# Kernel optimization log

Hardware: AMD Instinct MI355X
Metric: run time of the kernel (lower is better)

Reference implementation:

```python
import jax, jax.numpy as jnp
import numpy as np

SM_SCALE = 0.07216878364870322  # 1/sqrt(192)
PAGE_SIZE = 64


def setup_inputs() -> dict:
    key = jax.random.key(0)
    ks = jax.random.split(key, 6)
    B, Hq, Hkv = 32, 16, 1
    DN, DR, DV = 128, 64, 128
    NUM_PAGES, MAX_PAGES = 2048, 64
    return {
        "q": jax.random.normal(ks[0], (B, Hq, DN + DR), dtype=jnp.float32),
        "k_nope_buffer": jax.random.normal(ks[1], (NUM_PAGES, PAGE_SIZE, Hkv, DN), dtype=jnp.float32),
        "k_rope_buffer": jax.random.normal(ks[2], (NUM_PAGES, PAGE_SIZE, Hkv, DR), dtype=jnp.float32),
        "v_buffer": jax.random.normal(ks[3], (NUM_PAGES, PAGE_SIZE, Hkv, DV), dtype=jnp.float32),
        "seq_lens": jax.random.randint(ks[4], (B,), 1, MAX_PAGES * PAGE_SIZE + 1, dtype=jnp.int32),
        "block_table": jax.random.randint(ks[5], (B, MAX_PAGES), 0, NUM_PAGES, dtype=jnp.int32),
    }


def reference(q, k_nope_buffer, k_rope_buffer, v_buffer, seq_lens, block_table):
    B, Hq, _ = q.shape
    Hkv = k_nope_buffer.shape[2]
    dn = k_nope_buffer.shape[-1]
    dv = v_buffer.shape[-1]
    max_kv = block_table.shape[1] * PAGE_SIZE

    q_nope = q[:, :, :dn]            # (B, Hq, dn)
    q_rope = q[:, :, dn:]            # (B, Hq, dr)

    # Gather pages per batch: (B, max_pages, page, Hkv, d) -> (B, max_kv, Hkv, d)
    kn = k_nope_buffer[block_table].reshape(B, max_kv, Hkv, dn)
    kr = k_rope_buffer[block_table].reshape(B, max_kv, Hkv, -1)
    v = v_buffer[block_table].reshape(B, max_kv, Hkv, dv)

    rep = Hq // Hkv  # GQA repeat_interleave == repeat along head axis
    if rep != 1:
        kn = jnp.repeat(kn, rep, axis=2)
        kr = jnp.repeat(kr, rep, axis=2)
        v = jnp.repeat(v, rep, axis=2)

    scores = (jnp.einsum('bhd,bkhd->bhk', q_nope, kn)
              + jnp.einsum('bhd,bkhd->bhk', q_rope, kr)).astype(jnp.float32) * SM_SCALE
    # Mask out key positions beyond each sequence length (replaces per-batch slicing)
    valid = jnp.arange(max_kv)[None, None, :] < seq_lens[:, None, None]
    scores = jnp.where(valid, scores, -jnp.inf)
    probs = jax.nn.softmax(scores, axis=-1).astype(v.dtype)  # (B, Hq, max_kv)
    out = jnp.einsum('bhk,bkhd->bhd', probs, v)              # (B, Hq, dv)
    return out
```

## Files before the change

### kernel.cpp

```cpp
#include <hip/hip_runtime.h>
#include <math.h>

#define NB 32
#define HQ 16
#define DN 128
#define DR 64
#define DQ (DN + DR)
#define DV 128
#define PAGE 64
#define MAXP 64
#define SM_SCALE 0.07216878364870322f
#define RS 88

typedef __attribute__((ext_vector_type(8))) _Float16 f16x8;
typedef __attribute__((ext_vector_type(4))) _Float16 f16x4;
typedef __attribute__((ext_vector_type(2))) __fp16   h16x2;
typedef __attribute__((ext_vector_type(4))) float    f32x4;

union F16x8 { f16x8 v; h16x2 h[4]; };
union F16x4 { f16x4 v; h16x2 h[2]; };

#define WAVE_LDS_FENCE() asm volatile("s_waitcnt lgkmcnt(0)" ::: "memory")

template<int NSC>
__global__ __launch_bounds__(64, 1)
void attn_partial_kernel(const float* __restrict__ q,
                         const float* __restrict__ kn,
                         const float* __restrict__ kr,
                         const float* __restrict__ v,
                         const int* __restrict__ seq_lens,
                         const int* __restrict__ block_table,
                         float* __restrict__ o_part,
                         float* __restrict__ ml_part)
{
    const int lane = (int)threadIdx.x;
    const int ln   = lane & 15;
    const int qd   = lane >> 4;

    const int b = blockIdx.x / NSC;
    const int c = blockIdx.x % NSC;

    const int seq = seq_lens[b];
    if (c * PAGE >= seq) return;

    __shared__ _Float16 p_s[HQ][RS];

    F16x8 bq[6];
    {
        const float* qrow = q + ((size_t)b * HQ + ln) * DQ + qd * 8;
        #pragma unroll
        for (int kt = 0; kt < 6; kt++) {
            float4 x0 = *(const float4*)(qrow + kt * 32);
            float4 x1 = *(const float4*)(qrow + kt * 32 + 4);
            bq[kt].h[0] = __builtin_amdgcn_cvt_pkrtz(x0.x, x0.y);
            bq[kt].h[1] = __builtin_amdgcn_cvt_pkrtz(x0.z, x0.w);
            bq[kt].h[2] = __builtin_amdgcn_cvt_pkrtz(x1.x, x1.y);
            bq[kt].h[3] = __builtin_amdgcn_cvt_pkrtz(x1.z, x1.w);
        }
    }

    float m_run = -INFINITY, l_run = 0.f;
    f32x4 o_acc[8];
    #pragma unroll
    for (int i = 0; i < 8; i++) o_acc[i] = (f32x4){0.f, 0.f, 0.f, 0.f};

    #pragma unroll
    for (int pg = 0; pg < MAXP / NSC; pg++) {
        const int page = c + pg * NSC;
        if (page * PAGE >= seq) break;
        const int pid = block_table[b * MAXP + page];

        const float* knb = kn + (size_t)pid * PAGE * DN;
        const float* krb = kr + (size_t)pid * PAGE * DR;
        const float* vb  = v  + (size_t)pid * PAGE * DV;

        f32x4 sc[4];
        #pragma unroll
        for (int mt = 0; mt < 4; mt++) sc[mt] = (f32x4){0.f, 0.f, 0.f, 0.f};
        #pragma unroll
        for (int mt = 0; mt < 4; mt++) {
            const float* rn = knb + (mt * 16 + ln) * DN + qd * 8;
            const float* rr = krb + (mt * 16 + ln) * DR + qd * 8;
            #pragma unroll
            for (int kt = 0; kt < 6; kt++) {
                const float* src = (kt < 4) ? (rn + kt * 32) : (rr + (kt - 4) * 32);
                float4 x0 = *(const float4*)(src);
                float4 x1 = *(const float4*)(src + 4);
                F16x8 a;
                a.h[0] = __builtin_amdgcn_cvt_pkrtz(x0.x, x0.y);
                a.h[1] = __builtin_amdgcn_cvt_pkrtz(x0.z, x0.w);
                a.h[2] = __builtin_amdgcn_cvt_pkrtz(x1.x, x1.y);
                a.h[3] = __builtin_amdgcn_cvt_pkrtz(x1.z, x1.w);
                sc[mt] = __builtin_amdgcn_mfma_f32_16x16x32_f16(a.v, bq[kt].v, sc[mt], 0, 0, 0);
            }
        }

        float vraw[16][8];
        #pragma unroll
        for (int kt2 = 0; kt2 < 2; kt2++) {
            const int t0 = kt2 * 32 + qd * 8;
            #pragma unroll
            for (int mt2 = 0; mt2 < 8; mt2++) {
                const float* vc = vb + mt2 * 16 + ln;
                #pragma unroll
                for (int j = 0; j < 8; j++)
                    vraw[kt2 * 8 + mt2][j] = vc[(size_t)(t0 + j) * DV];
            }
        }

        float sv[4][4];
        float smax = -INFINITY;
        #pragma unroll
        for (int mt = 0; mt < 4; mt++)
            #pragma unroll
            for (int r = 0; r < 4; r++) {
                int tok = page * PAGE + mt * 16 + qd * 4 + r;
                float x = (tok < seq) ? sc[mt][r] * SM_SCALE : -INFINITY;
                sv[mt][r] = x;
                smax = fmaxf(smax, x);
            }
        smax = fmaxf(smax, __shfl_xor(smax, 16));
        smax = fmaxf(smax, __shfl_xor(smax, 32));
        const float m_new = fmaxf(m_run, smax);
        const float alpha = __expf(m_run - m_new);
        m_run = m_new;
        float lsum = 0.f;
        #pragma unroll
        for (int mt = 0; mt < 4; mt++)
            #pragma unroll
            for (int r = 0; r < 4; r++) {
                float e = __expf(sv[mt][r] - m_new);
                sv[mt][r] = e;
                lsum += e;
            }
        lsum += __shfl_xor(lsum, 16);
        lsum += __shfl_xor(lsum, 32);
        l_run = l_run * alpha + lsum;

        WAVE_LDS_FENCE();
        #pragma unroll
        for (int mt = 0; mt < 4; mt++) {
            F16x4 w;
            w.h[0] = __builtin_amdgcn_cvt_pkrtz(sv[mt][0], sv[mt][1]);
            w.h[1] = __builtin_amdgcn_cvt_pkrtz(sv[mt][2], sv[mt][3]);
            *(f16x4*)(&p_s[ln][mt * 16 + qd * 4]) = w.v;
        }
        WAVE_LDS_FENCE();

        #pragma unroll
        for (int i = 0; i < 8; i++) o_acc[i] *= alpha;

        #pragma unroll
        for (int kt2 = 0; kt2 < 2; kt2++) {
            f16x8 pf = *(const f16x8*)(&p_s[ln][kt2 * 32 + qd * 8]);
            #pragma unroll
            for (int mt2 = 0; mt2 < 8; mt2++) {
                const float* vr = vraw[kt2 * 8 + mt2];
                F16x8 a;
                a.h[0] = __builtin_amdgcn_cvt_pkrtz(vr[0], vr[1]);
                a.h[1] = __builtin_amdgcn_cvt_pkrtz(vr[2], vr[3]);
                a.h[2] = __builtin_amdgcn_cvt_pkrtz(vr[4], vr[5]);
                a.h[3] = __builtin_amdgcn_cvt_pkrtz(vr[6], vr[7]);
                o_acc[mt2] = __builtin_amdgcn_mfma_f32_16x16x32_f16(a.v, pf, o_acc[mt2], 0, 0, 0);
            }
        }
    }

    float* op = o_part + ((size_t)(b * NSC + c) * HQ + ln) * DV + qd * 4;
    #pragma unroll
    for (int mt2 = 0; mt2 < 8; mt2++)
        *(f32x4*)(op + mt2 * 16) = o_acc[mt2];
    if (qd == 0) {
        float2* ml = (float2*)(ml_part) + (size_t)(b * NSC + c) * HQ + ln;
        *ml = make_float2(m_run, l_run);
    }
}

template<int NSC>
__global__ __launch_bounds__(128)
void attn_combine_kernel(const float* __restrict__ o_part,
                         const float* __restrict__ ml_part,
                         const int* __restrict__ seq_lens,
                         float* __restrict__ out)
{
    const int h = blockIdx.x;
    const int b = blockIdx.y;
    const int d = (int)threadIdx.x;
    const int seq = seq_lens[b];
    int npages = (seq + PAGE - 1) / PAGE;
    int ns = npages < NSC ? npages : NSC;

    const float2* mlb = (const float2*)(ml_part) + (size_t)b * NSC * HQ + h;
    float M = -INFINITY;
    #pragma unroll 8
    for (int s2 = 0; s2 < ns; s2++)
        M = fmaxf(M, mlb[(size_t)s2 * HQ].x);

    float acc = 0.f, den = 0.f;
    #pragma unroll 4
    for (int s2 = 0; s2 < ns; s2++) {
        float2 ml = mlb[(size_t)s2 * HQ];
        float e = __expf(ml.x - M);
        float o = o_part[((size_t)(b * NSC + s2) * HQ + h) * DV + d];
        acc += e * o;
        den += e * ml.y;
    }
    out[((size_t)b * HQ + h) * DV + d] = acc / den;
}

template<int NSC>
static void launch_all(const float* q, const float* kn, const float* kr,
                       const float* v, const int* seq_lens, const int* block_table,
                       float* d_ws, float* d_out, hipStream_t stream)
{
    float* o_part  = d_ws;
    float* ml_part = o_part + (size_t)NB * NSC * HQ * DV;
    attn_partial_kernel<NSC><<<NB * NSC, 64, 0, stream>>>(
        q, kn, kr, v, seq_lens, block_table, o_part, ml_part);
    attn_combine_kernel<NSC><<<dim3(HQ, NB), 128, 0, stream>>>(
        o_part, ml_part, seq_lens, d_out);
}

extern "C" void kernel_launch(void* const* d_in, const int* in_sizes, int n_in,
                              void* d_out, int out_size, void* d_ws, size_t ws_size,
                              hipStream_t stream)
{
    const float* q  = (const float*)d_in[0];
    const float* kn = (const float*)d_in[1];
    const float* kr = (const float*)d_in[2];
    const float* v  = (const float*)d_in[3];
    const int* seq_lens    = (const int*)d_in[4];
    const int* block_table = (const int*)d_in[5];

    const size_t need64 = (size_t)NB * 64 * HQ * (DV + 2) * 4;
    const size_t need32 = (size_t)NB * 32 * HQ * (DV + 2) * 4;

    if (ws_size >= need64)
        launch_all<64>(q, kn, kr, v, seq_lens, block_table, (float*)d_ws, (float*)d_out, stream);
    else if (ws_size >= need32)
        launch_all<32>(q, kn, kr, v, seq_lens, block_table, (float*)d_ws, (float*)d_out, stream);
    else
        launch_all<16>(q, kn, kr, v, seq_lens, block_table, (float*)d_ws, (float*)d_out, stream);
}
```

Before: 185.1 us.

## Split attention into 32-token chunks per workgroup and drop online softmax loop

Each workgroup now processes a fixed sub-page chunk of tokens (32 by default) instead of a single page via a loop, doubling the number of split-KV partials. The online-softmax rescaling is removed since each workgroup sees one chunk, and V loads are issued before the QK MFMAs so they overlap. This increases parallelism and memory-level concurrency at the cost of twice as much partial-output traffic and more work in the combine kernel.

```diff
diff --git a/kernel.cpp b/kernel.cpp
--- a/kernel.cpp
+++ b/kernel.cpp
@@ -10,7 +10,6 @@
 #define PAGE 64
 #define MAXP 64
 #define SM_SCALE 0.07216878364870322f
-#define RS 88
 
 typedef __attribute__((ext_vector_type(8))) _Float16 f16x8;
 typedef __attribute__((ext_vector_type(4))) _Float16 f16x4;
@@ -22,7 +21,7 @@
 
 #define WAVE_LDS_FENCE() asm volatile("s_waitcnt lgkmcnt(0)" ::: "memory")
 
-template<int NSC>
+template<int MT>
 __global__ __launch_bounds__(64, 1)
 void attn_partial_kernel(const float* __restrict__ q,
                          const float* __restrict__ kn,
@@ -33,17 +32,29 @@
                          float* __restrict__ o_part,
                          float* __restrict__ ml_part)
 {
+    constexpr int NS  = (MAXP * PAGE) / (MT * 16);
+    constexpr int PRS = MT * 16 + 8;
+
     const int lane = (int)threadIdx.x;
     const int ln   = lane & 15;
     const int qd   = lane >> 4;
 
-    const int b = blockIdx.x / NSC;
-    const int c = blockIdx.x % NSC;
+    const int b = blockIdx.x / NS;
+    const int c = blockIdx.x % NS;
+    const int tok0 = c * (MT * 16);
 
     const int seq = seq_lens[b];
-    if (c * PAGE >= seq) return;
-
-    __shared__ _Float16 p_s[HQ][RS];
+    if (tok0 >= seq) return;
+
+    const int page    = tok0 / PAGE;
+    const int in_page = tok0 % PAGE;
+    const int pid = block_table[b * MAXP + page];
+
+    __shared__ _Float16 p_s[HQ][PRS];
+
+    const float* knb = kn + (size_t)pid * PAGE * DN;
+    const float* krb = kr + (size_t)pid * PAGE * DR;
+    const float* vb  = v  + (size_t)pid * PAGE * DV;
 
     F16x8 bq[6];
     {
@@ -59,138 +70,119 @@
         }
     }
 
-    float m_run = -INFINITY, l_run = 0.f;
+    float vraw[MT / 2 * 8][8];
+    #pragma unroll
+    for (int kt2 = 0; kt2 < MT / 2; kt2++) {
+        const int t0 = in_page + kt2 * 32 + qd * 8;
+        #pragma unroll
+        for (int mt2 = 0; mt2 < 8; mt2++) {
+            const float* vc = vb + mt2 * 16 + ln;
+            #pragma unroll
+            for (int j = 0; j < 8; j++)
+                vraw[kt2 * 8 + mt2][j] = vc[(size_t)(t0 + j) * DV];
+        }
+    }
+
+    f32x4 sc[MT];
+    #pragma unroll
+    for (int mt = 0; mt < MT; mt++) sc[mt] = (f32x4){0.f, 0.f, 0.f, 0.f};
+    #pragma unroll
+    for (int mt = 0; mt < MT; mt++) {
+        const float* rn = knb + (size_t)(in_page + mt * 16 + ln) * DN + qd * 8;
+        const float* rr = krb + (size_t)(in_page + mt * 16 + ln) * DR + qd * 8;
+        #pragma unroll
+        for (int kt = 0; kt < 6; kt++) {
+            const float* src = (kt < 4) ? (rn + kt * 32) : (rr + (kt - 4) * 32);
+            float4 x0 = *(const float4*)(src);
+            float4 x1 = *(const float4*)(src + 4);
+            F16x8 a;
+            a.h[0] = __builtin_amdgcn_cvt_pkrtz(x0.x, x0.y);
+            a.h[1] = __builtin_amdgcn_cvt_pkrtz(x0.z, x0.w);
+            a.h[2] = __builtin_amdgcn_cvt_pkrtz(x1.x, x1.y);
+            a.h[3] = __builtin_amdgcn_cvt_pkrtz(x1.z, x1.w);
+            sc[mt] = __builtin_amdgcn_mfma_f32_16x16x32_f16(a.v, bq[kt].v, sc[mt], 0, 0, 0);
+        }
+    }
+
+    float sv[MT][4];
+    float smax = -INFINITY;
+    #pragma unroll
+    for (int mt = 0; mt < MT; mt++)
+        #pragma unroll
+        for (int r = 0; r < 4; r++) {
+            int tok = tok0 + mt * 16 + qd * 4 + r;
+            float x = (tok < seq) ? sc[mt][r] * SM_SCALE : -INFINITY;
+            sv[mt][r] = x;
+            smax = fmaxf(smax, x);
+        }
+    smax = fmaxf(smax, __shfl_xor(smax, 16));
+    smax = fmaxf(smax, __shfl_xor(smax, 32));
+    float lsum = 0.f;
+    #pragma unroll
+    for (int mt = 0; mt < MT; mt++)
+        #pragma unroll
+        for (int r = 0; r < 4; r++) {
+            float e = __expf(sv[mt][r] - smax);
+            sv[mt][r] = e;
+            lsum += e;
+        }
+    lsum += __shfl_xor(lsum, 16);
+    lsum += __shfl_xor(lsum, 32);
+
+    #pragma unroll
+    for (int mt = 0; mt < MT; mt++) {
+        F16x4 w;
+        w.h[0] = __builtin_amdgcn_cvt_pkrtz(sv[mt][0], sv[mt][1]);
+        w.h[1] = __builtin_amdgcn_cvt_pkrtz(sv[mt][2], sv[mt][3]);
+        *(f16x4*)(&p_s[ln][mt * 16 + qd * 4]) = w.v;
+    }
+    WAVE_LDS_FENCE();
+
     f32x4 o_acc[8];
     #pragma unroll
     for (int i = 0; i < 8; i++) o_acc[i] = (f32x4){0.f, 0.f, 0.f, 0.f};
-
-    #pragma unroll
-    for (int pg = 0; pg < MAXP / NSC; pg++) {
-        const int page = c + pg * NSC;
-        if (page * PAGE >= seq) break;
-        const int pid = block_table[b * MAXP + page];
-
-        const float* knb = kn + (size_t)pid * PAGE * DN;
-        const float* krb = kr + (size_t)pid * PAGE * DR;
-        const float* vb  = v  + (size_t)pid * PAGE * DV;
-
-        f32x4 sc[4];
-        #pragma unroll
-        for (int mt = 0; mt < 4; mt++) sc[mt] = (f32x4){0.f, 0.f, 0.f, 0.f};
-        #pragma unroll
-        for (int mt = 0; mt < 4; mt++) {
-            const float* rn = knb + (mt * 16 + ln) * DN + qd * 8;
-            const float* rr = krb + (mt * 16 + ln) * DR + qd * 8;
-            #pragma unroll
-            for (int kt = 0; kt < 6; kt++) {
-                const float* src = (kt < 4) ? (rn + kt * 32) : (rr + (kt - 4) * 32);
-                float4 x0 = *(const float4*)(src);
-                float4 x1 = *(const float4*)(src + 4);
-                F16x8 a;
-                a.h[0] = __builtin_amdgcn_cvt_pkrtz(x0.x, x0.y);
-                a.h[1] = __builtin_amdgcn_cvt_pkrtz(x0.z, x0.w);
-                a.h[2] = __builtin_amdgcn_cvt_pkrtz(x1.x, x1.y);
-                a.h[3] = __builtin_amdgcn_cvt_pkrtz(x1.z, x1.w);
-                sc[mt] = __builtin_amdgcn_mfma_f32_16x16x32_f16(a.v, bq[kt].v, sc[mt], 0, 0, 0);
-            }
-        }
-
-        float vraw[16][8];
-        #pragma unroll
-        for (int kt2 = 0; kt2 < 2; kt2++) {
-            const int t0 = kt2 * 32 + qd * 8;
-            #pragma unroll
-            for (int mt2 = 0; mt2 < 8; mt2++) {
-                const float* vc = vb + mt2 * 16 + ln;
-                #pragma unroll
-                for (int j = 0; j < 8; j++)
-                    vraw[kt2 * 8 + mt2][j] = vc[(size_t)(t0 + j) * DV];
-            }
-        }
-
-        float sv[4][4];
-        float smax = -INFINITY;
-        #pragma unroll
-        for (int mt = 0; mt < 4; mt++)
-            #pragma unroll
-            for (int r = 0; r < 4; r++) {
-                int tok = page * PAGE + mt * 16 + qd * 4 + r;
-                float x = (tok < seq) ? sc[mt][r] * SM_SCALE : -INFINITY;
-                sv[mt][r] = x;
-                smax = fmaxf(smax, x);
-            }
-        smax = fmaxf(smax, __shfl_xor(smax, 16));
-        smax = fmaxf(smax, __shfl_xor(smax, 32));
-        const float m_new = fmaxf(m_run, smax);
-        const float alpha = __expf(m_run - m_new);
-        m_run = m_new;
-        float lsum = 0.f;
-        #pragma unroll
-        for (int mt = 0; mt < 4; mt++)
-            #pragma unroll
-            for (int r = 0; r < 4; r++) {
-                float e = __expf(sv[mt][r] - m_new);
-                sv[mt][r] = e;
-                lsum += e;
-            }
-        lsum += __shfl_xor(lsum, 16);
-        lsum += __shfl_xor(lsum, 32);
-        l_run = l_run * alpha + lsum;
-
-        WAVE_LDS_FENCE();
-        #pragma unroll
-        for (int mt = 0; mt < 4; mt++) {
-            F16x4 w;
-            w.h[0] = __builtin_amdgcn_cvt_pkrtz(sv[mt][0], sv[mt][1]);
-            w.h[1] = __builtin_amdgcn_cvt_pkrtz(sv[mt][2], sv[mt][3]);
-            *(f16x4*)(&p_s[ln][mt * 16 + qd * 4]) = w.v;
-        }
-        WAVE_LDS_FENCE();
-
-        #pragma unroll
-        for (int i = 0; i < 8; i++) o_acc[i] *= alpha;
-
-        #pragma unroll
-        for (int kt2 = 0; kt2 < 2; kt2++) {
-            f16x8 pf = *(const f16x8*)(&p_s[ln][kt2 * 32 + qd * 8]);
-            #pragma unroll
-            for (int mt2 = 0; mt2 < 8; mt2++) {
-                const float* vr = vraw[kt2 * 8 + mt2];
-                F16x8 a;
-                a.h[0] = __builtin_amdgcn_cvt_pkrtz(vr[0], vr[1]);
-                a.h[1] = __builtin_amdgcn_cvt_pkrtz(vr[2], vr[3]);
-                a.h[2] = __builtin_amdgcn_cvt_pkrtz(vr[4], vr[5]);
-                a.h[3] = __builtin_amdgcn_cvt_pkrtz(vr[6], vr[7]);
-                o_acc[mt2] = __builtin_amdgcn_mfma_f32_16x16x32_f16(a.v, pf, o_acc[mt2], 0, 0, 0);
-            }
-        }
-    }
-
-    float* op = o_part + ((size_t)(b * NSC + c) * HQ + ln) * DV + qd * 4;
+    #pragma unroll
+    for (int kt2 = 0; kt2 < MT / 2; kt2++) {
+        f16x8 pf = *(const f16x8*)(&p_s[ln][kt2 * 32 + qd * 8]);
+        #pragma unroll
+        for (int mt2 = 0; mt2 < 8; mt2++) {
+            const float* vr = vraw[kt2 * 8 + mt2];
+            F16x8 a;
+            a.h[0] = __builtin_amdgcn_cvt_pkrtz(vr[0], vr[1]);
+            a.h[1] = __builtin_amdgcn_cvt_pkrtz(vr[2], vr[3]);
+            a.h[2] = __builtin_amdgcn_cvt_pkrtz(vr[4], vr[5]);
+            a.h[3] = __builtin_amdgcn_cvt_pkrtz(vr[6], vr[7]);
+            o_acc[mt2] = __builtin_amdgcn_mfma_f32_16x16x32_f16(a.v, pf, o_acc[mt2], 0, 0, 0);
+        }
+    }
+
+    float* op = o_part + ((size_t)(b * NS + c) * HQ + ln) * DV + qd * 4;
     #pragma unroll
     for (int mt2 = 0; mt2 < 8; mt2++)
         *(f32x4*)(op + mt2 * 16) = o_acc[mt2];
     if (qd == 0) {
-        float2* ml = (float2*)(ml_part) + (size_t)(b * NSC + c) * HQ + ln;
-        *ml = make_float2(m_run, l_run);
-    }
-}
-
-template<int NSC>
+        float2* ml = (float2*)(ml_part) + (size_t)(b * NS + c) * HQ + ln;
+        *ml = make_float2(smax, lsum);
+    }
+}
+
+template<int MT>
 __global__ __launch_bounds__(128)
 void attn_combine_kernel(const float* __restrict__ o_part,
                          const float* __restrict__ ml_part,
                          const int* __restrict__ seq_lens,
                          float* __restrict__ out)
 {
+    constexpr int NS  = (MAXP * PAGE) / (MT * 16);
+    constexpr int TPC = MT * 16;
     const int h = blockIdx.x;
     const int b = blockIdx.y;
     const int d = (int)threadIdx.x;
     const int seq = seq_lens[b];
-    int npages = (seq + PAGE - 1) / PAGE;
-    int ns = npages < NSC ? npages : NSC;
-
-    const float2* mlb = (const float2*)(ml_part) + (size_t)b * NSC * HQ + h;
+    int ns = (seq + TPC - 1) / TPC;
+    if (ns > NS) ns = NS;
+
+    const float2* mlb = (const float2*)(ml_part) + (size_t)b * NS * HQ + h;
     float M = -INFINITY;
     #pragma unroll 8
     for (int s2 = 0; s2 < ns; s2++)
@@ -201,23 +193,24 @@
     for (int s2 = 0; s2 < ns; s2++) {
         float2 ml = mlb[(size_t)s2 * HQ];
         float e = __expf(ml.x - M);
-        float o = o_part[((size_t)(b * NSC + s2) * HQ + h) * DV + d];
+        float o = o_part[((size_t)(b * NS + s2) * HQ + h) * DV + d];
         acc += e * o;
         den += e * ml.y;
     }
     out[((size_t)b * HQ + h) * DV + d] = acc / den;
 }
 
-template<int NSC>
+template<int MT>
 static void launch_all(const float* q, const float* kn, const float* kr,
                        const float* v, const int* seq_lens, const int* block_table,
                        float* d_ws, float* d_out, hipStream_t stream)
 {
+    constexpr int NS = (MAXP * PAGE) / (MT * 16);
     float* o_part  = d_ws;
-    float* ml_part = o_part + (size_t)NB * NSC * HQ * DV;
-    attn_partial_kernel<NSC><<<NB * NSC, 64, 0, stream>>>(
+    float* ml_part = o_part + (size_t)NB * NS * HQ * DV;
+    attn_partial_kernel<MT><<<NB * NS, 64, 0, stream>>>(
         q, kn, kr, v, seq_lens, block_table, o_part, ml_part);
-    attn_combine_kernel<NSC><<<dim3(HQ, NB), 128, 0, stream>>>(
+    attn_combine_kernel<MT><<<dim3(HQ, NB), 128, 0, stream>>>(
         o_part, ml_part, seq_lens, d_out);
 }
 
@@ -232,13 +225,9 @@
     const int* seq_lens    = (const int*)d_in[4];
     const int* block_table = (const int*)d_in[5];
 
-    const size_t need64 = (size_t)NB * 64 * HQ * (DV + 2) * 4;
-    const size_t need32 = (size_t)NB * 32 * HQ * (DV + 2) * 4;
-
-    if (ws_size >= need64)
-        launch_all<64>(q, kn, kr, v, seq_lens, block_table, (float*)d_ws, (float*)d_out, stream);
-    else if (ws_size >= need32)
-        launch_all<32>(q, kn, kr, v, seq_lens, block_table, (float*)d_ws, (float*)d_out, stream);
+    const size_t need128 = (size_t)NB * 128 * HQ * (DV + 2) * 4;
+    if (ws_size >= need128)
+        launch_all<2>(q, kn, kr, v, seq_lens, block_table, (float*)d_ws, (float*)d_out, stream);
     else
-        launch_all<16>(q, kn, kr, v, seq_lens, block_table, (float*)d_ws, (float*)d_out, stream);
-}
+        launch_all<4>(q, kn, kr, v, seq_lens, block_table, (float*)d_ws, (float*)d_out, stream);
+}
```

New measurement: 200.4 us. 1.08x slower.

## Software-pipeline K/V loads in bands and interleave with score MFMAs

Applied to the files above, without the earlier changes.

Restructures the per-page loop so K loads come in two bands of two row tiles and V loads in two halves. Score MFMAs on the first band overlap with the outstanding loads of the next band, with compiler barriers pinning the issue order. The block_table lookup for the first page is hoisted above the early exit, and q conversion is deferred until after the first loads are issued. It also makes page assignment per split contiguous instead of strided and shrinks the LDS row stride; the risk is higher register pressure, since two K bands and two V bands are live at once.

```diff
diff --git a/kernel.cpp b/kernel.cpp
--- a/kernel.cpp
+++ b/kernel.cpp
@@ -10,7 +10,7 @@
 #define PAGE 64
 #define MAXP 64
 #define SM_SCALE 0.07216878364870322f
-#define RS 88
+#define RS 72
 
 typedef __attribute__((ext_vector_type(8))) _Float16 f16x8;
 typedef __attribute__((ext_vector_type(4))) _Float16 f16x4;
@@ -20,9 +20,77 @@
 union F16x8 { f16x8 v; h16x2 h[4]; };
 union F16x4 { f16x4 v; h16x2 h[2]; };
 
+#define SCHED_PIN()      asm volatile("" ::: "memory")
 #define WAVE_LDS_FENCE() asm volatile("s_waitcnt lgkmcnt(0)" ::: "memory")
 
-template<int NSC>
+
+static __device__ __forceinline__ void issue_k_band(
+    const float* knb, const float* krb, int mtbase, int ln, int qd, float4* kb)
+{
+    #pragma unroll
+    for (int m = 0; m < 2; m++) {
+        const int mt = mtbase + m;
+        const float* rn = knb + (size_t)(mt * 16 + ln) * DN + qd * 8;
+        const float* rr = krb + (size_t)(mt * 16 + ln) * DR + qd * 8;
+        #pragma unroll
+        for (int kt = 0; kt < 4; kt++) {
+            kb[m * 12 + kt * 2]     = *(const float4*)(rn + kt * 32);
+            kb[m * 12 + kt * 2 + 1] = *(const float4*)(rn + kt * 32 + 4);
+        }
+        kb[m * 12 + 8]  = *(const float4*)(rr);
+        kb[m * 12 + 9]  = *(const float4*)(rr + 4);
+        kb[m * 12 + 10] = *(const float4*)(rr + 32);
+        kb[m * 12 + 11] = *(const float4*)(rr + 36);
+    }
+}
+
+static __device__ __forceinline__ void issue_v_band(
+    const float* vb, int kt2, int ln, int qd, float vr[8][8])
+{
+    const int t0 = kt2 * 32 + qd * 8;
+    #pragma unroll
+    for (int mt2 = 0; mt2 < 8; mt2++) {
+        const float* vc = vb + mt2 * 16 + ln;
+        #pragma unroll
+        for (int j = 0; j < 8; j++)
+            vr[mt2][j] = vc[(size_t)(t0 + j) * DV];
+    }
+}
+
+static __device__ __forceinline__ void score_band(
+    const float4* kb, const F16x8* bq, int mtbase, f32x4* sc)
+{
+    #pragma unroll
+    for (int m = 0; m < 2; m++)
+        #pragma unroll
+        for (int kt = 0; kt < 6; kt++) {
+            float4 x0 = kb[m * 12 + kt * 2];
+            float4 x1 = kb[m * 12 + kt * 2 + 1];
+            F16x8 a;
+            a.h[0] = __builtin_amdgcn_cvt_pkrtz(x0.x, x0.y);
+            a.h[1] = __builtin_amdgcn_cvt_pkrtz(x0.z, x0.w);
+            a.h[2] = __builtin_amdgcn_cvt_pkrtz(x1.x, x1.y);
+            a.h[3] = __builtin_amdgcn_cvt_pkrtz(x1.z, x1.w);
+            sc[mtbase + m] = __builtin_amdgcn_mfma_f32_16x16x32_f16(
+                a.v, bq[kt].v, sc[mtbase + m], 0, 0, 0);
+        }
+}
+
+static __device__ __forceinline__ void pv_band(
+    const float vr[8][8], f16x8 pf, f32x4* o_acc)
+{
+    #pragma unroll
+    for (int mt2 = 0; mt2 < 8; mt2++) {
+        F16x8 a;
+        a.h[0] = __builtin_amdgcn_cvt_pkrtz(vr[mt2][0], vr[mt2][1]);
+        a.h[1] = __builtin_amdgcn_cvt_pkrtz(vr[mt2][2], vr[mt2][3]);
+        a.h[2] = __builtin_amdgcn_cvt_pkrtz(vr[mt2][4], vr[mt2][5]);
+        a.h[3] = __builtin_amdgcn_cvt_pkrtz(vr[mt2][6], vr[mt2][7]);
+        o_acc[mt2] = __builtin_amdgcn_mfma_f32_16x16x32_f16(a.v, pf, o_acc[mt2], 0, 0, 0);
+    }
+}
+
+template<int PPC>
 __global__ __launch_bounds__(64, 1)
 void attn_partial_kernel(const float* __restrict__ q,
                          const float* __restrict__ kn,
@@ -33,6 +101,7 @@
                          float* __restrict__ o_part,
                          float* __restrict__ ml_part)
 {
+    constexpr int NSC = MAXP / PPC;
     const int lane = (int)threadIdx.x;
     const int ln   = lane & 15;
     const int qd   = lane >> 4;
@@ -41,72 +110,67 @@
     const int c = blockIdx.x % NSC;
 
     const int seq = seq_lens[b];
-    if (c * PAGE >= seq) return;
+    int pid = block_table[b * MAXP + c * PPC];
+    if (c * PPC * PAGE >= seq) return;
 
     __shared__ _Float16 p_s[HQ][RS];
 
-    F16x8 bq[6];
+    float4 qraw[12];
     {
         const float* qrow = q + ((size_t)b * HQ + ln) * DQ + qd * 8;
         #pragma unroll
         for (int kt = 0; kt < 6; kt++) {
-            float4 x0 = *(const float4*)(qrow + kt * 32);
-            float4 x1 = *(const float4*)(qrow + kt * 32 + 4);
-            bq[kt].h[0] = __builtin_amdgcn_cvt_pkrtz(x0.x, x0.y);
-            bq[kt].h[1] = __builtin_amdgcn_cvt_pkrtz(x0.z, x0.w);
-            bq[kt].h[2] = __builtin_amdgcn_cvt_pkrtz(x1.x, x1.y);
-            bq[kt].h[3] = __builtin_amdgcn_cvt_pkrtz(x1.z, x1.w);
-        }
-    }
-
+            qraw[2 * kt]     = *(const float4*)(qrow + kt * 32);
+            qraw[2 * kt + 1] = *(const float4*)(qrow + kt * 32 + 4);
+        }
+    }
+
+    F16x8 bq[6];
     float m_run = -INFINITY, l_run = 0.f;
     f32x4 o_acc[8];
     #pragma unroll
     for (int i = 0; i < 8; i++) o_acc[i] = (f32x4){0.f, 0.f, 0.f, 0.f};
 
     #pragma unroll
-    for (int pg = 0; pg < MAXP / NSC; pg++) {
-        const int page = c + pg * NSC;
+    for (int pg = 0; pg < PPC; pg++) {
+        const int page = c * PPC + pg;
         if (page * PAGE >= seq) break;
-        const int pid = block_table[b * MAXP + page];
+        if (pg > 0) pid = block_table[b * MAXP + page];
 
         const float* knb = kn + (size_t)pid * PAGE * DN;
         const float* krb = kr + (size_t)pid * PAGE * DR;
         const float* vb  = v  + (size_t)pid * PAGE * DV;
 
-        f32x4 sc[4];
-        #pragma unroll
-        for (int mt = 0; mt < 4; mt++) sc[mt] = (f32x4){0.f, 0.f, 0.f, 0.f};
-        #pragma unroll
-        for (int mt = 0; mt < 4; mt++) {
-            const float* rn = knb + (mt * 16 + ln) * DN + qd * 8;
-            const float* rr = krb + (mt * 16 + ln) * DR + qd * 8;
+        float4 kb0[24], kb1[24];
+        float  va[8][8], vbr[8][8];
+
+        issue_k_band(knb, krb, 0, ln, qd, kb0);
+        issue_v_band(vb, 0, ln, qd, va);
+        SCHED_PIN();
+
+        if (pg == 0) {
             #pragma unroll
             for (int kt = 0; kt < 6; kt++) {
-                const float* src = (kt < 4) ? (rn + kt * 32) : (rr + (kt - 4) * 32);
-                float4 x0 = *(const float4*)(src);
-                float4 x1 = *(const float4*)(src + 4);
-                F16x8 a;
-                a.h[0] = __builtin_amdgcn_cvt_pkrtz(x0.x, x0.y);
-                a.h[1] = __builtin_amdgcn_cvt_pkrtz(x0.z, x0.w);
-                a.h[2] = __builtin_amdgcn_cvt_pkrtz(x1.x, x1.y);
-                a.h[3] = __builtin_amdgcn_cvt_pkrtz(x1.z, x1.w);
-                sc[mt] = __builtin_amdgcn_mfma_f32_16x16x32_f16(a.v, bq[kt].v, sc[mt], 0, 0, 0);
+                float4 x0 = qraw[2 * kt], x1 = qraw[2 * kt + 1];
+                bq[kt].h[0] = __builtin_amdgcn_cvt_pkrtz(x0.x, x0.y);
+                bq[kt].h[1] = __builtin_amdgcn_cvt_pkrtz(x0.z, x0.w);
+                bq[kt].h[2] = __builtin_amdgcn_cvt_pkrtz(x1.x, x1.y);
+                bq[kt].h[3] = __builtin_amdgcn_cvt_pkrtz(x1.z, x1.w);
             }
         }
 
-        float vraw[16][8];
-        #pragma unroll
-        for (int kt2 = 0; kt2 < 2; kt2++) {
-            const int t0 = kt2 * 32 + qd * 8;
-            #pragma unroll
-            for (int mt2 = 0; mt2 < 8; mt2++) {
-                const float* vc = vb + mt2 * 16 + ln;
-                #pragma unroll
-                for (int j = 0; j < 8; j++)
-                    vraw[kt2 * 8 + mt2][j] = vc[(size_t)(t0 + j) * DV];
-            }
-        }
+        f32x4 sc[4];
+        #pragma unroll
+        for (int mt = 0; mt < 4; mt++) sc[mt] = (f32x4){0.f, 0.f, 0.f, 0.f};
+
+        score_band(kb0, bq, 0, sc);
+
+        issue_k_band(knb, krb, 2, ln, qd, kb1);
+        SCHED_PIN();
+        score_band(kb1, bq, 2, sc);
+
+        issue_v_band(vb, 1, ln, qd, vbr);
+        SCHED_PIN();
 
         float sv[4][4];
         float smax = -INFINITY;
@@ -150,19 +214,11 @@
         #pragma unroll
         for (int i = 0; i < 8; i++) o_acc[i] *= alpha;
 
-        #pragma unroll
-        for (int kt2 = 0; kt2 < 2; kt2++) {
-            f16x8 pf = *(const f16x8*)(&p_s[ln][kt2 * 32 + qd * 8]);
-            #pragma unroll
-            for (int mt2 = 0; mt2 < 8; mt2++) {
-                const float* vr = vraw[kt2 * 8 + mt2];
-                F16x8 a;
-                a.h[0] = __builtin_amdgcn_cvt_pkrtz(vr[0], vr[1]);
-                a.h[1] = __builtin_amdgcn_cvt_pkrtz(vr[2], vr[3]);
-                a.h[2] = __builtin_amdgcn_cvt_pkrtz(vr[4], vr[5]);
-                a.h[3] = __builtin_amdgcn_cvt_pkrtz(vr[6], vr[7]);
-                o_acc[mt2] = __builtin_amdgcn_mfma_f32_16x16x32_f16(a.v, pf, o_acc[mt2], 0, 0, 0);
-            }
+        {
+            f16x8 pf0 = *(const f16x8*)(&p_s[ln][qd * 8]);
+            pv_band(va, pf0, o_acc);
+            f16x8 pf1 = *(const f16x8*)(&p_s[ln][32 + qd * 8]);
+            pv_band(vbr, pf1, o_acc);
         }
     }
 
@@ -176,19 +232,21 @@
     }
 }
 
-template<int NSC>
+template<int PPC>
 __global__ __launch_bounds__(128)
 void attn_combine_kernel(const float* __restrict__ o_part,
                          const float* __restrict__ ml_part,
                          const int* __restrict__ seq_lens,
                          float* __restrict__ out)
 {
+    constexpr int NSC = MAXP / PPC;
+    constexpr int TPC = PPC * PAGE;
     const int h = blockIdx.x;
     const int b = blockIdx.y;
     const int d = (int)threadIdx.x;
     const int seq = seq_lens[b];
-    int npages = (seq + PAGE - 1) / PAGE;
-    int ns = npages < NSC ? npages : NSC;
+    int ns = (seq + TPC - 1) / TPC;
+    if (ns > NSC) ns = NSC;
 
     const float2* mlb = (const float2*)(ml_part) + (size_t)b * NSC * HQ + h;
     float M = -INFINITY;
@@ -208,16 +266,17 @@
     out[((size_t)b * HQ + h) * DV + d] = acc / den;
 }
 
-template<int NSC>
+template<int PPC>
 static void launch_all(const float* q, const float* kn, const float* kr,
                        const float* v, const int* seq_lens, const int* block_table,
                        float* d_ws, float* d_out, hipStream_t stream)
 {
+    constexpr int NSC = MAXP / PPC;
     float* o_part  = d_ws;
     float* ml_part = o_part + (size_t)NB * NSC * HQ * DV;
-    attn_partial_kernel<NSC><<<NB * NSC, 64, 0, stream>>>(
+    attn_partial_kernel<PPC><<<NB * NSC, 64, 0, stream>>>(
         q, kn, kr, v, seq_lens, block_table, o_part, ml_part);
-    attn_combine_kernel<NSC><<<dim3(HQ, NB), 128, 0, stream>>>(
+    attn_combine_kernel<PPC><<<dim3(HQ, NB), 128, 0, stream>>>(
         o_part, ml_part, seq_lens, d_out);
 }
 
@@ -232,13 +291,13 @@
     const int* seq_lens    = (const int*)d_in[4];
     const int* block_table = (const int*)d_in[5];
 
-    const size_t need64 = (size_t)NB * 64 * HQ * (DV + 2) * 4;
-    const size_t need32 = (size_t)NB * 32 * HQ * (DV + 2) * 4;
-
-    if (ws_size >= need64)
-        launch_all<64>(q, kn, kr, v, seq_lens, block_table, (float*)d_ws, (float*)d_out, stream);
-    else if (ws_size >= need32)
-        launch_all<32>(q, kn, kr, v, seq_lens, block_table, (float*)d_ws, (float*)d_out, stream);
+    const size_t need1 = (size_t)NB * 64 * HQ * (DV + 2) * 4;
+    const size_t need2 = (size_t)NB * 32 * HQ * (DV + 2) * 4;
+
+    if (ws_size >= need1)
+        launch_all<1>(q, kn, kr, v, seq_lens, block_table, (float*)d_ws, (float*)d_out, stream);
+    else if (ws_size >= need2)
+        launch_all<2>(q, kn, kr, v, seq_lens, block_table, (float*)d_ws, (float*)d_out, stream);
     else
-        launch_all<16>(q, kn, kr, v, seq_lens, block_table, (float*)d_ws, (float*)d_out, stream);
-}
+        launch_all<4>(q, kn, kr, v, seq_lens, block_table, (float*)d_ws, (float*)d_out, stream);
+}
```

After: 185.1 us. Within noise of the previous version (-0.0%).
